# Kernel tuning notes

Measured on AMD Instinct MI355X. Metric: run time of the kernel, lower is better.

Reference implementation:

```python
import jax, jax.numpy as jnp
import numpy as np

B, LQ, LK, D = 16, 2048, 2048, 64
TEMPERATURE = 8.0


def setup_inputs() -> dict:
    key = jax.random.key(0)
    kq, kk, kv, kt, km = jax.random.split(key, 5)
    q = jax.random.normal(kq, (B, LQ, D), dtype=jnp.float32)
    k = jax.random.normal(kk, (B, LK, D), dtype=jnp.float32)
    v = jax.random.normal(kv, (B, LK, D), dtype=jnp.float32)
    # time differences are positive
    time_diff = jax.random.uniform(kt, (B, LQ, LK), dtype=jnp.float32)
    mask = jax.random.randint(km, (B, LQ, LK), 0, 2).astype(bool)
    time_plus_weight = jnp.zeros((1,), dtype=jnp.float32)
    time_mul_weight = jnp.ones((1,), dtype=jnp.float32)
    return {"q": q, "k": k, "v": v, "time_diff": time_diff, "mask": mask,
            "time_plus_weight": time_plus_weight, "time_mul_weight": time_mul_weight}


def reference(q, k, v, time_diff, mask, time_plus_weight, time_mul_weight):
    # attn = QK^T / temperature  -> [B, LQ, LK]
    attn = jnp.einsum("bqd,bkd->bqk", q, k) / TEMPERATURE
    # time-decay bias (global mean/max over the whole time_diff tensor)
    td = time_diff / jnp.mean(time_diff)
    td = td + jax.nn.softplus(time_plus_weight) * jnp.max(td)
    time_diff_weight = 1.0 / jnp.log(jnp.exp(jnp.float32(1.0)) + td)
    attn = attn + time_mul_weight * time_diff_weight
    attn = jnp.where(mask, jnp.float32(-1e10), attn)
    attn = jax.nn.softmax(attn, axis=2)
    # dropout is identity in eval / p-effective-0 reference
    output = jnp.einsum("bqk,bkd->bqd", attn, v)
    return (output, attn)
```

## Files before the change

### kernel.cpp

```cpp
#include <hip/hip_runtime.h>
#include <hip/hip_bf16.h>

#define B_N 16
#define LQ_N 2048
#define LK_N 2048
#define D_N 64

typedef __attribute__((ext_vector_type(8))) __bf16 bf16x8;
typedef __attribute__((ext_vector_type(4))) float f32x4;
typedef __attribute__((ext_vector_type(2))) unsigned u32x2;
typedef __attribute__((ext_vector_type(4))) unsigned u32x4;

__device__ __forceinline__ unsigned cvt_pk_bf16(float lo, float hi) {
  unsigned r;
  asm("v_cvt_pk_bf16_f32 %0, %1, %2" : "=v"(r) : "v"(lo), "v"(hi));
  return r;
}

__device__ __forceinline__ void gl_lds16(const float* g, float* l) {
  __builtin_amdgcn_global_load_lds(
      (const __attribute__((address_space(1))) void*)g,
      (__attribute__((address_space(3))) void*)l, 16, 0, 0);
}

#define WAIT_VM0()   do { asm volatile("s_waitcnt vmcnt(0)" ::: "memory");  __builtin_amdgcn_sched_barrier(0); } while (0)
#define WAIT_VM4()   do { asm volatile("s_waitcnt vmcnt(4)" ::: "memory");  __builtin_amdgcn_sched_barrier(0); } while (0)
#define WAIT_LGKM0() do { asm volatile("s_waitcnt lgkmcnt(0)" ::: "memory"); __builtin_amdgcn_sched_barrier(0); } while (0)

__global__ __launch_bounds__(256) void red1_kernel(const float* __restrict__ td,
                                                   float* __restrict__ ws) {
  const int tid = threadIdx.x;
  const int gid = blockIdx.x * 256 + tid;
  float s = 0.f, mx = -1e30f;
  const float4* p = reinterpret_cast<const float4*>(td);
  for (int i = gid; i < 16777216; i += 524288) {
    float4 x = p[i];
    s += (x.x + x.y) + (x.z + x.w);
    mx = fmaxf(mx, fmaxf(fmaxf(x.x, x.y), fmaxf(x.z, x.w)));
  }
#pragma unroll
  for (int m = 1; m < 64; m <<= 1) {
    s += __shfl_xor(s, m, 64);
    mx = fmaxf(mx, __shfl_xor(mx, m, 64));
  }
  __shared__ float ss[4], sm[4];
  if ((tid & 63) == 0) { ss[tid >> 6] = s; sm[tid >> 6] = mx; }
  __syncthreads();
  if (tid == 0) {
    ws[blockIdx.x]        = (ss[0] + ss[1]) + (ss[2] + ss[3]);
    ws[2048 + blockIdx.x] = fmaxf(fmaxf(sm[0], sm[1]), fmaxf(sm[2], sm[3]));
  }
}

__global__ __launch_bounds__(256) void red2_kernel(const float* __restrict__ tpw,
                                                   const unsigned* __restrict__ mku,
                                                   float* __restrict__ ws) {
  const int tid = threadIdx.x;
  double s = 0.0; float mx = -1e30f;
  for (int i = tid; i < 2048; i += 256) { s += (double)ws[i]; mx = fmaxf(mx, ws[2048 + i]); }
#pragma unroll
  for (int m = 1; m < 64; m <<= 1) {
    s += __shfl_xor(s, m, 64);
    mx = fmaxf(mx, __shfl_xor(mx, m, 64));
  }
  unsigned big = 0;
  for (int i = tid; i < 1024; i += 256) big |= (mku[i] > 1u) ? 1u : 0u;
  const int anyw = __any(big != 0);
  __shared__ double sd[4]; __shared__ float sm[4]; __shared__ int sa[4];
  if ((tid & 63) == 0) { sd[tid >> 6] = s; sm[tid >> 6] = mx; sa[tid >> 6] = anyw; }
  __syncthreads();
  if (tid == 0) {
    double tot = (sd[0] + sd[1]) + (sd[2] + sd[3]);
    float m4 = fmaxf(fmaxf(sm[0], sm[1]), fmaxf(sm[2], sm[3]));
    double mean = tot / 67108864.0;
    float inv_mean = (float)(1.0 / mean);
    float sp = log1pf(__expf(tpw[0]));
    ws[4096] = inv_mean;
    ws[4097] = sp * m4 * inv_mean;
    ws[4098] = (sa[0] | sa[1] | sa[2] | sa[3]) ? 1.f : 0.f;
  }
}

__global__ __launch_bounds__(512, 6) void attn_kernel(
    const float* __restrict__ q, const float* __restrict__ kp, const float* __restrict__ vp,
    const float* __restrict__ td, const unsigned char* __restrict__ maskb,
    const float* __restrict__ tmwp, const float* __restrict__ ws,
    float* __restrict__ out, float* __restrict__ attn) {

  __shared__ float regA[8][1024];
  __shared__ float Qs[16 * 68];
  __shared__ unsigned short Ps[8][16 * 24];
  __shared__ float rsum[8][16];

  const int tid  = threadIdx.x;
  const int w    = tid >> 6;
  const int lane = tid & 63;
  const int lrow = lane & 15;
  const int lgrp = lane >> 4;

  const int b     = blockIdx.x >> 7;
  const int qbase = (blockIdx.x & 127) << 4;

  const float inv_mean = ws[4096];
  const float bias_c   = ws[4097];
  const float tmw      = tmwp[0];
  const int   msh      = (ws[4098] != 0.f) ? 0 : 2;

  {
    const int g = tid * 2, row = g >> 6, col = g & 63;
    const float* qp0 = q + ((size_t)(b * LQ_N + qbase + row) << 6) + col;
    Qs[row * 68 + col]     = qp0[0] * 0.125f;
    Qs[row * 68 + col + 1] = qp0[1] * 0.125f;
  }
  __syncthreads();

  bf16x8 qa[2];
#pragma unroll
  for (int h = 0; h < 2; ++h) {
    f32x4 a0 = *(const f32x4*)&Qs[lrow * 68 + h * 32 + lgrp * 8];
    f32x4 a1 = *(const f32x4*)&Qs[lrow * 68 + h * 32 + lgrp * 8 + 4];
    u32x4 kd = { cvt_pk_bf16(a0[0], a0[1]), cvt_pk_bf16(a0[2], a0[3]),
                 cvt_pk_bf16(a1[0], a1[1]), cvt_pk_bf16(a1[2], a1[3]) };
    qa[h] = __builtin_bit_cast(bf16x8, kd);
  }

  const size_t kvb = (size_t)b << 17;

  auto dma16 = [&](const float* src_base, int c) {
#pragma unroll
    for (int t = 0; t < 4; ++t) {
      const int row  = t * 4 + lgrp;
      const int slot = lrow;
      const float* src = src_base + kvb +
          ((size_t)(c * 128 + w * 16 + row) << 6) + ((slot ^ (row & 7)) << 2);
      gl_lds16(src, &regA[w][t * 256]);
    }
  };

  dma16(kp, 0);
  float rs[4] = {0.f, 0.f, 0.f, 0.f};
  u32x2 E[16];

#pragma unroll
  for (int c = 0; c < 16; ++c) {
    WAIT_VM0();
    f32x4 acc = {0.f, 0.f, 0.f, 0.f};
#pragma unroll
    for (int h = 0; h < 2; ++h) {
      const int g0 = (h * 8 + lgrp * 2 + 0) ^ (lrow & 7);
      const int g1 = (h * 8 + lgrp * 2 + 1) ^ (lrow & 7);
      f32x4 ka = *(const f32x4*)&regA[w][lrow * 64 + g0 * 4];
      f32x4 kc = *(const f32x4*)&regA[w][lrow * 64 + g1 * 4];
      u32x4 kd = { cvt_pk_bf16(ka[0], ka[1]), cvt_pk_bf16(ka[2], ka[3]),
                   cvt_pk_bf16(kc[0], kc[1]), cvt_pk_bf16(kc[2], kc[3]) };
      acc = __builtin_amdgcn_mfma_f32_16x16x32_bf16(qa[h], __builtin_bit_cast(bf16x8, kd),
                                                    acc, 0, 0, 0);
    }
    WAIT_LGKM0();
    if (c < 15) dma16(kp, c + 1);

    const int jg = c * 128 + w * 16 + lrow;
    const size_t offb = ((size_t)(b * LQ_N + qbase + lgrp * 4) << 11) + jg;
    float e4[4];
#pragma unroll
    for (int i = 0; i < 4; ++i) {
      const size_t off = offb + ((size_t)i << 11);
      const float tdv = __builtin_nontemporal_load(td + off);
      const unsigned char mk = __builtin_nontemporal_load(maskb + (off << msh));
      const float wgt = tmw * __fdividef(1.f, __logf(2.718281828f + tdv * inv_mean + bias_c));
      const float sv = acc[i] + wgt;
      const float e = mk ? 0.f : __expf(sv);
      e4[i] = e;
      rs[i] += e;
    }
    E[c] = u32x2{ cvt_pk_bf16(e4[0], e4[1]), cvt_pk_bf16(e4[2], e4[3]) };
  }

#pragma unroll
  for (int m = 1; m < 16; m <<= 1)
#pragma unroll
    for (int i = 0; i < 4; ++i) rs[i] += __shfl_xor(rs[i], m, 64);
  if (lrow == 0) {
#pragma unroll
    for (int i = 0; i < 4; ++i) rsum[w][lgrp * 4 + i] = rs[i];
  }
  __syncthreads();
  float invl[4];
#pragma unroll
  for (int i = 0; i < 4; ++i) {
    float s = 0.f;
#pragma unroll
    for (int w2 = 0; w2 < 8; ++w2) s += rsum[w2][lgrp * 4 + i];
    invl[i] = __fdividef(1.f, s);
  }

  f32x4 oacc[4];
#pragma unroll
  for (int n = 0; n < 4; ++n) oacc[n] = {0.f, 0.f, 0.f, 0.f};
  dma16(vp, 0);

  const u32x4 zz = {0u, 0u, 0u, 0u};
#pragma unroll
  for (int c = 0; c < 16; ++c) {
    if (c == 0) { WAIT_VM0(); } else { WAIT_VM4(); }

    const unsigned ex = E[c][0], ey = E[c][1];
    float p4[4];
    p4[0] = __uint_as_float(ex << 16)          * invl[0];
    p4[1] = __uint_as_float(ex & 0xffff0000u)  * invl[1];
    p4[2] = __uint_as_float(ey << 16)          * invl[2];
    p4[3] = __uint_as_float(ey & 0xffff0000u)  * invl[3];

    const unsigned d01 = cvt_pk_bf16(p4[0], p4[1]);
    const unsigned d23 = cvt_pk_bf16(p4[2], p4[3]);
    Ps[w][(lgrp * 4 + 0) * 24 + lrow] = (unsigned short)(d01 & 0xffffu);
    Ps[w][(lgrp * 4 + 1) * 24 + lrow] = (unsigned short)(d01 >> 16);
    Ps[w][(lgrp * 4 + 2) * 24 + lrow] = (unsigned short)(d23 & 0xffffu);
    Ps[w][(lgrp * 4 + 3) * 24 + lrow] = (unsigned short)(d23 >> 16);

    bf16x8 pa;
    if (lgrp < 2) pa = *(const bf16x8*)&Ps[w][lrow * 24 + lgrp * 8];
    else          pa = __builtin_bit_cast(bf16x8, zz);

#pragma unroll
    for (int n = 0; n < 4; ++n) {
      u32x4 vd;
      if (lgrp < 2) {
        float vv[8];
#pragma unroll
        for (int e = 0; e < 8; ++e) {
          const int r    = lgrp * 8 + e;
          const int dcol = n * 16 + lrow;
          const int slot = (dcol >> 2) ^ (r & 7);
          vv[e] = regA[w][r * 64 + slot * 4 + (dcol & 3)];
        }
        vd = u32x4{ cvt_pk_bf16(vv[0], vv[1]), cvt_pk_bf16(vv[2], vv[3]),
                    cvt_pk_bf16(vv[4], vv[5]), cvt_pk_bf16(vv[6], vv[7]) };
      } else {
        vd = zz;
      }
      oacc[n] = __builtin_amdgcn_mfma_f32_16x16x32_bf16(pa, __builtin_bit_cast(bf16x8, vd),
                                                        oacc[n], 0, 0, 0);
    }

    WAIT_LGKM0();
    if (c < 15) dma16(vp, c + 1);

    const int jg = c * 128 + w * 16 + lrow;
    const size_t offb = ((size_t)(b * LQ_N + qbase + lgrp * 4) << 11) + jg;
#pragma unroll
    for (int i = 0; i < 4; ++i)
      __builtin_nontemporal_store(p4[i], attn + offb + ((size_t)i << 11));
  }

#pragma unroll
  for (int n = 0; n < 4; ++n)
#pragma unroll
    for (int i = 0; i < 4; ++i)
      regA[w][(lgrp * 4 + i) * 64 + n * 16 + lrow] = oacc[n][i];
  __syncthreads();
  for (int i2 = tid; i2 < 1024; i2 += 512) {
    float s = 0.f;
#pragma unroll
    for (int w2 = 0; w2 < 8; ++w2) s += regA[w2][i2];
    out[((size_t)(b * LQ_N + qbase) << 6) + i2] = s;
  }
}

extern "C" void kernel_launch(void* const* d_in, const int* in_sizes, int n_in,
                              void* d_out, int out_size, void* d_ws, size_t ws_size,
                              hipStream_t stream) {
  const float* q   = (const float*)d_in[0];
  const float* k   = (const float*)d_in[1];
  const float* v   = (const float*)d_in[2];
  const float* td  = (const float*)d_in[3];
  const unsigned char* mask = (const unsigned char*)d_in[4];
  const float* tpw = (const float*)d_in[5];
  const float* tmw = (const float*)d_in[6];
  float* out  = (float*)d_out;
  float* attn = out + (size_t)B_N * LQ_N * D_N;
  float* wsf  = (float*)d_ws;

  red1_kernel<<<2048, 256, 0, stream>>>(td, wsf);
  red2_kernel<<<1, 256, 0, stream>>>(tpw, (const unsigned*)mask, wsf);
  attn_kernel<<<2048, 512, 0, stream>>>(q, k, v, td, mask, tmw, wsf, out, attn);
}
```

Measured before the change: 391.5 us.

## Double-buffer K/V LDS tiles and prefetch time_diff/mask one chunk ahead

Doubles the per-wave LDS staging buffer so the K and V chunk DMAs run two chunks ahead instead of one, with vmcnt waits adjusted to match. It also loads the time_diff and mask values for the next chunk into registers before the current chunk's softmax math, and issues the first V prefetches before the row-sum reduction. The goal is to hide global memory latency behind compute. In exchange it uses more LDS and registers, so the launch-bounds occupancy hint drops from 6 to 4 blocks, and correctness now depends on the hand-tuned vmcnt counts.

```diff
diff --git a/kernel.cpp b/kernel.cpp
--- a/kernel.cpp
+++ b/kernel.cpp
@@ -23,9 +23,8 @@
       (__attribute__((address_space(3))) void*)l, 16, 0, 0);
 }
 
-#define WAIT_VM0()   do { asm volatile("s_waitcnt vmcnt(0)" ::: "memory");  __builtin_amdgcn_sched_barrier(0); } while (0)
-#define WAIT_VM4()   do { asm volatile("s_waitcnt vmcnt(4)" ::: "memory");  __builtin_amdgcn_sched_barrier(0); } while (0)
-#define WAIT_LGKM0() do { asm volatile("s_waitcnt lgkmcnt(0)" ::: "memory"); __builtin_amdgcn_sched_barrier(0); } while (0)
+#define WAIT_VMC(N)  do { asm volatile("s_waitcnt vmcnt(" #N ")" ::: "memory"); __builtin_amdgcn_sched_barrier(0); } while (0)
+#define WAIT_LGKM0() do { asm volatile("s_waitcnt lgkmcnt(0)" ::: "memory");    __builtin_amdgcn_sched_barrier(0); } while (0)
 
 __global__ __launch_bounds__(256) void red1_kernel(const float* __restrict__ td,
                                                    float* __restrict__ ws) {
@@ -81,13 +80,13 @@
   }
 }
 
-__global__ __launch_bounds__(512, 6) void attn_kernel(
+__global__ __launch_bounds__(512, 4) void attn_kernel(
     const float* __restrict__ q, const float* __restrict__ kp, const float* __restrict__ vp,
     const float* __restrict__ td, const unsigned char* __restrict__ maskb,
     const float* __restrict__ tmwp, const float* __restrict__ ws,
     float* __restrict__ out, float* __restrict__ attn) {
 
-  __shared__ float regA[8][1024];
+  __shared__ float regA[8][2][1024];
   __shared__ float Qs[16 * 68];
   __shared__ unsigned short Ps[8][16 * 24];
   __shared__ float rsum[8][16];
@@ -126,47 +125,62 @@
 
   const size_t kvb = (size_t)b << 17;
 
-  auto dma16 = [&](const float* src_base, int c) {
+  auto dma16 = [&](const float* src_base, int c, int pb) {
 #pragma unroll
     for (int t = 0; t < 4; ++t) {
       const int row  = t * 4 + lgrp;
       const int slot = lrow;
       const float* src = src_base + kvb +
           ((size_t)(c * 128 + w * 16 + row) << 6) + ((slot ^ (row & 7)) << 2);
-      gl_lds16(src, &regA[w][t * 256]);
+      gl_lds16(src, &regA[w][pb][t * 256]);
     }
   };
 
-  dma16(kp, 0);
+  auto ldtd = [&](int c, float* tdv, unsigned* mkv) {
+    const int jg = c * 128 + w * 16 + lrow;
+    const size_t offb = ((size_t)(b * LQ_N + qbase + lgrp * 4) << 11) + jg;
+#pragma unroll
+    for (int i = 0; i < 4; ++i) {
+      const size_t off = offb + ((size_t)i << 11);
+      tdv[i] = __builtin_nontemporal_load(td + off);
+      mkv[i] = maskb[off << msh];
+    }
+  };
+
+  dma16(kp, 0, 0);
+  dma16(kp, 1, 1);
+  float    tdbuf[2][4];
+  unsigned mkbuf[2][4];
+  ldtd(0, tdbuf[0], mkbuf[0]);
+
   float rs[4] = {0.f, 0.f, 0.f, 0.f};
   u32x2 E[16];
 
 #pragma unroll
   for (int c = 0; c < 16; ++c) {
-    WAIT_VM0();
+    if (c == 15) { WAIT_VMC(8); } else { WAIT_VMC(12); }
+
     f32x4 acc = {0.f, 0.f, 0.f, 0.f};
 #pragma unroll
     for (int h = 0; h < 2; ++h) {
       const int g0 = (h * 8 + lgrp * 2 + 0) ^ (lrow & 7);
       const int g1 = (h * 8 + lgrp * 2 + 1) ^ (lrow & 7);
-      f32x4 ka = *(const f32x4*)&regA[w][lrow * 64 + g0 * 4];
-      f32x4 kc = *(const f32x4*)&regA[w][lrow * 64 + g1 * 4];
+      f32x4 ka = *(const f32x4*)&regA[w][c & 1][lrow * 64 + g0 * 4];
+      f32x4 kc = *(const f32x4*)&regA[w][c & 1][lrow * 64 + g1 * 4];
       u32x4 kd = { cvt_pk_bf16(ka[0], ka[1]), cvt_pk_bf16(ka[2], ka[3]),
                    cvt_pk_bf16(kc[0], kc[1]), cvt_pk_bf16(kc[2], kc[3]) };
       acc = __builtin_amdgcn_mfma_f32_16x16x32_bf16(qa[h], __builtin_bit_cast(bf16x8, kd),
                                                     acc, 0, 0, 0);
     }
     WAIT_LGKM0();
-    if (c < 15) dma16(kp, c + 1);
-
-    const int jg = c * 128 + w * 16 + lrow;
-    const size_t offb = ((size_t)(b * LQ_N + qbase + lgrp * 4) << 11) + jg;
+    if (c < 14) dma16(kp, c + 2, c & 1);
+    if (c < 15) ldtd(c + 1, tdbuf[(c + 1) & 1], mkbuf[(c + 1) & 1]);
+
     float e4[4];
 #pragma unroll
     for (int i = 0; i < 4; ++i) {
-      const size_t off = offb + ((size_t)i << 11);
-      const float tdv = __builtin_nontemporal_load(td + off);
-      const unsigned char mk = __builtin_nontemporal_load(maskb + (off << msh));
+      const float tdv = tdbuf[c & 1][i];
+      const unsigned mk = mkbuf[c & 1][i];
       const float wgt = tmw * __fdividef(1.f, __logf(2.718281828f + tdv * inv_mean + bias_c));
       const float sv = acc[i] + wgt;
       const float e = mk ? 0.f : __expf(sv);
@@ -176,6 +190,9 @@
     E[c] = u32x2{ cvt_pk_bf16(e4[0], e4[1]), cvt_pk_bf16(e4[2], e4[3]) };
   }
 
+  dma16(vp, 0, 0);
+  dma16(vp, 1, 1);
+
 #pragma unroll
   for (int m = 1; m < 16; m <<= 1)
 #pragma unroll
@@ -197,19 +214,21 @@
   f32x4 oacc[4];
 #pragma unroll
   for (int n = 0; n < 4; ++n) oacc[n] = {0.f, 0.f, 0.f, 0.f};
-  dma16(vp, 0);
 
   const u32x4 zz = {0u, 0u, 0u, 0u};
 #pragma unroll
   for (int c = 0; c < 16; ++c) {
-    if (c == 0) { WAIT_VM0(); } else { WAIT_VM4(); }
+    if (c == 0)       { WAIT_VMC(4);  }
+    else if (c == 1)  { WAIT_VMC(8);  }
+    else if (c == 15) { WAIT_VMC(8);  }
+    else              { WAIT_VMC(12); }
 
     const unsigned ex = E[c][0], ey = E[c][1];
     float p4[4];
-    p4[0] = __uint_as_float(ex << 16)          * invl[0];
-    p4[1] = __uint_as_float(ex & 0xffff0000u)  * invl[1];
-    p4[2] = __uint_as_float(ey << 16)          * invl[2];
-    p4[3] = __uint_as_float(ey & 0xffff0000u)  * invl[3];
+    p4[0] = __uint_as_float(ex << 16)         * invl[0];
+    p4[1] = __uint_as_float(ex & 0xffff0000u) * invl[1];
+    p4[2] = __uint_as_float(ey << 16)         * invl[2];
+    p4[3] = __uint_as_float(ey & 0xffff0000u) * invl[3];
 
     const unsigned d01 = cvt_pk_bf16(p4[0], p4[1]);
     const unsigned d23 = cvt_pk_bf16(p4[2], p4[3]);
@@ -232,7 +251,7 @@
           const int r    = lgrp * 8 + e;
           const int dcol = n * 16 + lrow;
           const int slot = (dcol >> 2) ^ (r & 7);
-          vv[e] = regA[w][r * 64 + slot * 4 + (dcol & 3)];
+          vv[e] = regA[w][c & 1][r * 64 + slot * 4 + (dcol & 3)];
         }
         vd = u32x4{ cvt_pk_bf16(vv[0], vv[1]), cvt_pk_bf16(vv[2], vv[3]),
                     cvt_pk_bf16(vv[4], vv[5]), cvt_pk_bf16(vv[6], vv[7]) };
@@ -244,7 +263,7 @@
     }
 
     WAIT_LGKM0();
-    if (c < 15) dma16(vp, c + 1);
+    if (c < 14) dma16(vp, c + 2, c & 1);
 
     const int jg = c * 128 + w * 16 + lrow;
     const size_t offb = ((size_t)(b * LQ_N + qbase + lgrp * 4) << 11) + jg;
@@ -257,12 +276,12 @@
   for (int n = 0; n < 4; ++n)
 #pragma unroll
     for (int i = 0; i < 4; ++i)
-      regA[w][(lgrp * 4 + i) * 64 + n * 16 + lrow] = oacc[n][i];
+      regA[w][0][(lgrp * 4 + i) * 64 + n * 16 + lrow] = oacc[n][i];
   __syncthreads();
   for (int i2 = tid; i2 < 1024; i2 += 512) {
     float s = 0.f;
 #pragma unroll
-    for (int w2 = 0; w2 < 8; ++w2) s += regA[w2][i2];
+    for (int w2 = 0; w2 < 8; ++w2) s += regA[w2][0][i2];
     out[((size_t)(b * LQ_N + qbase) << 6) + i2] = s;
   }
 }
```

After: 345.5 us. 11.8% less time.
